# Optimization experiments

Hardware: AMD Instinct MI355X
Metric: run time of the kernel (lower is better)

Reference implementation:

```python
import jax, jax.numpy as jnp
import numpy as np


def _ln(x, g, b, eps=1e-5):
    m = jnp.mean(x, axis=-1, keepdims=True)
    v = jnp.var(x, axis=-1, keepdims=True)  # biased var, matches torch LayerNorm
    return (x - m) / jnp.sqrt(v + eps) * g + b


def setup_inputs() -> dict:
    key = jax.random.key(0)
    ks = jax.random.split(key, 10)
    B, S, T, D, F = 4, 8, 1024, 768, 16
    inp = {
        "target_hidden": jax.random.normal(ks[0], (B, T, D), jnp.float32),
        "support_hidden": jax.random.normal(ks[1], (B, S, T, D), jnp.float32),
        "support_token_mask": jax.random.bernoulli(ks[2], 0.8, (B, S, T)),
        "support_features": jax.random.normal(ks[3], (B, T, F), jnp.float32),
        # LayerNorm params
        "t_g": jnp.ones((D,), jnp.float32), "t_b": jnp.zeros((D,), jnp.float32),
        "s_g": jnp.ones((D,), jnp.float32), "s_b": jnp.zeros((D,), jnp.float32),
        "o_g": jnp.ones((D,), jnp.float32), "o_b": jnp.zeros((D,), jnp.float32),
        # score MLP: Linear(2D->D), GELU, Linear(D->1)
        "score_w1": jax.random.normal(ks[4], (2 * D, D), jnp.float32) * 0.02,
        "score_b1": jnp.zeros((D,), jnp.float32),
        "score_w2": jax.random.normal(ks[5], (D, 1), jnp.float32) * 0.02,
        "score_b2": jnp.zeros((1,), jnp.float32),
        # gate MLP: Linear(2D+F->D), GELU, Linear(D->1), Sigmoid
        "gate_w1": jax.random.normal(ks[6], (2 * D + F, D), jnp.float32) * 0.02,
        "gate_b1": jnp.zeros((D,), jnp.float32),
        "gate_w2": jax.random.normal(ks[7], (D, 1), jnp.float32) * 0.02,
        "gate_b2": jnp.zeros((1,), jnp.float32),
    }
    return inp


def reference(target_hidden, support_hidden, support_token_mask, support_features,
              t_g, t_b, s_g, s_b, o_g, o_b,
              score_w1, score_b1, score_w2, score_b2,
              gate_w1, gate_b1, gate_w2, gate_b2):
    D = target_hidden.shape[-1]
    mask = support_token_mask  # (B,S,T) bool

    th = _ln(target_hidden, t_g, t_b)        # (B,T,D)
    sh = _ln(support_hidden, s_g, s_b)       # (B,S,T,D)

    # score MLP on concat([target_expanded, support], -1) == split-weight form
    h = (jnp.einsum('btd,df->btf', th, score_w1[:D])[:, None, :, :]
         + jnp.einsum('bstd,df->bstf', sh, score_w1[D:]) + score_b1)  # (B,S,T,D)
    h = jax.nn.gelu(h, approximate=False)
    scores = jnp.einsum('bstd,d->bst', h, score_w2[:, 0]) + score_b2[0]  # (B,S,T)

    scores = jnp.where(mask, scores, -10000.0)
    w = jax.nn.softmax(scores, axis=1)
    w = w * mask.astype(w.dtype)
    w = w / jnp.clip(jnp.sum(w, axis=1, keepdims=True), 1e-8)

    summary = jnp.einsum('bst,bstd->btd', w, sh)  # (B,T,D)
    has_support = jnp.any(mask, axis=1)           # (B,T)
    summary = jnp.where(has_support[..., None], summary, 0.0)

    gcat = jnp.concatenate([th, summary, support_features], axis=-1)  # (B,T,2D+F)
    g = jax.nn.gelu(gcat @ gate_w1 + gate_b1, approximate=False)
    gate = jax.nn.sigmoid(g @ gate_w2 + gate_b2)  # (B,T,1)

    fused = gate * summary + (1.0 - gate) * th    # dropout is identity in eval
    out = _ln(th + fused, o_g, o_b)
    return out, gate.squeeze(-1)
```

## Files before the change

kernel.cpp:

```cpp
#include <hip/hip_runtime.h>
#include <hip/hip_bf16.h>

#define D768 768

typedef __attribute__((ext_vector_type(8))) short short8;
typedef __attribute__((ext_vector_type(4))) float f32x4;

__device__ __forceinline__ unsigned short f2bf(float f){
  union { float f; unsigned u; } v; v.f = f;
  unsigned r = v.u + 0x7FFFu + ((v.u >> 16) & 1u);
  return (unsigned short)(r >> 16);
}
__device__ __forceinline__ float bf2f(unsigned short u){
  union { unsigned u; float f; } v; v.u = ((unsigned)u) << 16;
  return v.f;
}
__device__ __forceinline__ float gelu_f(float x){
  float y = fabsf(x) * 0.7071067811865475f;
  float t = __builtin_amdgcn_rcpf(fmaf(0.3275911f, y, 1.0f));
  float p = fmaf(fmaf(fmaf(fmaf(1.061405429f, t, -1.453152027f), t, 1.421413741f),
                      t, -0.284496736f), t, 0.254829592f) * t;
  float e = __expf(-y * y);
  float erf_abs = fmaf(-p, e, 1.0f);
  float erfv = copysignf(erf_abs, x);
  return 0.5f * x * (1.0f + erfv);
}
__device__ __forceinline__ void gload16(const void* g, void* l){
  __builtin_amdgcn_global_load_lds((const __attribute__((address_space(1))) void*)g,
                                   (__attribute__((address_space(3))) void*)l, 16, 0, 0);
}

__global__ __launch_bounds__(256)
void k_mega(const float* __restrict__ target, const float* __restrict__ support,
            const float* __restrict__ t_g, const float* __restrict__ t_b,
            const float* __restrict__ s_g, const float* __restrict__ s_b,
            float* __restrict__ th, unsigned short* __restrict__ gcat,
            unsigned short* __restrict__ sh,
            const float* __restrict__ sw1, const float* __restrict__ gw1,
            unsigned short* __restrict__ WtA, unsigned short* __restrict__ WtB,
            unsigned short* __restrict__ WtG,
            float* __restrict__ scores, const float* __restrict__ sb2,
            float* __restrict__ gacc, const float* __restrict__ gb2,
            const unsigned char* __restrict__ m, int* __restrict__ flag){
  int blk = blockIdx.x;
  int t = threadIdx.x;
  if (blk < 128){
    int i = blk * 256 + t;
    if (i < 32768) scores[i] = sb2[0];
    if (i < 4096)  gacc[i]   = gb2[0];
    if (blk == 0){
      __shared__ int s;
      if (t == 0) s = 0;
      __syncthreads();
      int nz = 0;
      for (int j = t; j < 2048; j += 256) nz += (m[4*j+1] != 0);
      atomicAdd(&s, nz);
      __syncthreads();
      if (t == 0) *flag = (s == 0) ? 1 : 0;
    }
    return;
  }
  if (blk < 2456){
    int tile = blk - 128;
    const float* W; unsigned short* Wt; int Kin, Kpad;
    if (tile < 576)      { W = sw1;              Wt = WtA; Kin = 768;  Kpad = 768;  }
    else if (tile < 1152){ W = sw1 + 768ull*768; Wt = WtB; Kin = 768;  Kpad = 768;  tile -= 576; }
    else                 { W = gw1;              Wt = WtG; Kin = 1552; Kpad = 1568; tile -= 1152; }
    int ntk = Kpad >> 5;
    int k0 = (tile % ntk) << 5, n0 = (tile / ntk) << 5;
    __shared__ float ts[32][33];
    int tx = t & 31, ty = t >> 5;
    #pragma unroll
    for (int r = 0; r < 4; ++r){
      int k = k0 + ty + r*8;
      ts[ty + r*8][tx] = (k < Kin) ? W[(size_t)k * D768 + n0 + tx] : 0.f;
    }
    __syncthreads();
    #pragma unroll
    for (int r = 0; r < 4; ++r){
      int n = n0 + ty + r*8;
      Wt[(size_t)n * Kpad + k0 + tx] = f2bf(ts[tx][ty + r*8]);
    }
    return;
  }
  bool isT = blk < 3480;
  int row = (isT ? (blk - 2456) : (blk - 3480)) * 4 + (t >> 6);
  int lane = t & 63;
  const float* xr = (isT ? target : support) + (size_t)row * D768;
  float4 v0 = *(const float4*)(xr + lane*4);
  float4 v1 = *(const float4*)(xr + 256 + lane*4);
  float4 v2 = *(const float4*)(xr + 512 + lane*4);
  float s  = v0.x+v0.y+v0.z+v0.w + v1.x+v1.y+v1.z+v1.w + v2.x+v2.y+v2.z+v2.w;
  float ss = v0.x*v0.x+v0.y*v0.y+v0.z*v0.z+v0.w*v0.w
           + v1.x*v1.x+v1.y*v1.y+v1.z*v1.z+v1.w*v1.w
           + v2.x*v2.x+v2.y*v2.y+v2.z*v2.z+v2.w*v2.w;
  #pragma unroll
  for (int o = 32; o; o >>= 1){ s += __shfl_xor(s, o); ss += __shfl_xor(ss, o); }
  float mean = s * (1.f/768.f);
  float var  = ss * (1.f/768.f) - mean*mean;
  float rstd = rsqrtf(var + 1e-5f);
  const float* gg = isT ? t_g : s_g;
  const float* bb = isT ? t_b : s_b;
  #pragma unroll
  for (int k = 0; k < 3; ++k){
    int c = lane*4 + k*256;
    float4 v = (k==0) ? v0 : (k==1) ? v1 : v2;
    float4 gv = *(const float4*)(gg + c);
    float4 bv = *(const float4*)(bb + c);
    float o0 = (v.x-mean)*rstd*gv.x + bv.x;
    float o1 = (v.y-mean)*rstd*gv.y + bv.y;
    float o2 = (v.z-mean)*rstd*gv.z + bv.z;
    float o3 = (v.w-mean)*rstd*gv.w + bv.w;
    ushort4 ub; ub.x=f2bf(o0); ub.y=f2bf(o1); ub.z=f2bf(o2); ub.w=f2bf(o3);
    if (isT){
      float4 ov; ov.x=o0; ov.y=o1; ov.z=o2; ov.w=o3;
      *(float4*)(th + (size_t)row * D768 + c) = ov;
      *(ushort4*)(gcat + (size_t)row * 1568 + c) = ub;
    } else {
      *(ushort4*)(sh + (size_t)row * D768 + c) = ub;
    }
  }
}

template<int MODE, int BN>
__launch_bounds__(256)
__global__ void k_gemm(const unsigned short* __restrict__ A, int lda,
                       const unsigned short* __restrict__ Bt, int ldb,
                       int ksteps, int ntn,
                       const float* __restrict__ tproj,
                       const float* __restrict__ b1,
                       const float* __restrict__ w2,
                       float* __restrict__ out){
  constexpr int NJ  = BN / 32;
  constexpr int BCH = BN / 64;
  __shared__ __align__(16) unsigned short As[3][128*32];
  __shared__ __align__(16) unsigned short Bs[3][BN*32];
  const int cpx = gridDim.x >> 3;
  const int logical = ((int)blockIdx.x & 7) * cpx + ((int)blockIdx.x >> 3);
  const int m0 = (logical / ntn) * 128, n0 = (logical % ntn) * BN;
  const int t = threadIdx.x, lane = t & 63, w = t >> 6;
  const int wrow = (w >> 1) * 64, wcol = (w & 1) * (BN/2);
  const int lo16 = lane & 15;
  const int hs = ((lane >> 4) ^ ((lo16 >> 1) & 3)) * 8;
  const int crow = lane >> 2;
  const int cseg = (((lane & 3) ^ ((lane >> 3) & 3)) * 8);
  const unsigned short* ga = A  + (size_t)(m0 + w*32 + crow) * lda + cseg;
  const unsigned short* gb = Bt + (size_t)(n0 + w*(BN/4) + crow) * ldb + cseg;
  f32x4 acc[4][NJ] = {};

#define STAGEK(BUF, KS) do {                                                   \
    const unsigned short* gak_ = ga + (size_t)(KS)*32;                         \
    const unsigned short* gbk_ = gb + (size_t)(KS)*32;                         \
    _Pragma("unroll")                                                          \
    for (int c = 0; c < 2; ++c)                                                \
      gload16(gak_ + (size_t)(c*16)*lda, &As[BUF][w*1024 + c*512]);            \
    _Pragma("unroll")                                                          \
    for (int c = 0; c < BCH; ++c)                                              \
      gload16(gbk_ + (size_t)(c*16)*ldb, &Bs[BUF][w*(BN/4)*32 + c*512]);       \
  } while (0)

#define COMPUTEK(BUF) do {                                                     \
    const unsigned short* pa_ = &As[BUF][(wrow + lo16)*32 + hs];               \
    const unsigned short* pb_ = &Bs[BUF][(wcol + lo16)*32 + hs];               \
    short8 af_[4], bf_[NJ];                                                    \
    _Pragma("unroll")                                                          \
    for (int i = 0; i < 4; ++i) af_[i] = *(const short8*)(pa_ + i*16*32);      \
    _Pragma("unroll")                                                          \
    for (int j = 0; j < NJ; ++j) bf_[j] = *(const short8*)(pb_ + j*16*32);     \
    __builtin_amdgcn_s_setprio(1);                                             \
    _Pragma("unroll")                                                          \
    for (int i = 0; i < 4; ++i)                                                \
      _Pragma("unroll")                                                        \
      for (int j = 0; j < NJ; ++j)                                             \
        acc[i][j] = __builtin_amdgcn_mfma_f32_16x16x32_bf16(af_[i], bf_[j], acc[i][j], 0, 0, 0); \
    __builtin_amdgcn_s_setprio(0);                                             \
  } while (0)

#define WAITN(n) asm volatile("s_waitcnt vmcnt(" #n ")" ::: "memory")

  {
    int pro = ksteps < 2 ? ksteps : 2;
    for (int p = 0; p < pro; ++p) STAGEK(p, p);
  }
  for (int ks = 0; ks < ksteps; ++ks){
    int rem = ksteps - ks;
    if (rem >= 2){ if constexpr (BCH == 2) WAITN(4); else WAITN(3); }
    else WAITN(0);
    __builtin_amdgcn_s_barrier();
    __builtin_amdgcn_sched_barrier(0);
    if (ks + 2 < ksteps) STAGEK((ks + 2) % 3, ks + 2);
    COMPUTEK(ks % 3);
  }
#undef STAGEK
#undef COMPUTEK
#undef WAITN

  if (MODE == 0){
    #pragma unroll
    for (int i = 0; i < 4; ++i)
      #pragma unroll
      for (int reg = 0; reg < 4; ++reg){
        int row = m0 + wrow + i*16 + ((lane >> 4) << 2) + reg;
        float* orow = out + (size_t)row * D768 + n0 + wcol + (lane & 15);
        #pragma unroll
        for (int j = 0; j < NJ; ++j) orow[j*16] = acc[i][j][reg];
      }
  } else {
    #pragma unroll
    for (int i = 0; i < 4; ++i)
      #pragma unroll
      for (int reg = 0; reg < 4; ++reg){
        int row = m0 + wrow + i*16 + ((lane >> 4) << 2) + reg;
        const float* tp = nullptr;
        if (MODE == 1){
          int trow = ((row >> 13) << 10) | (row & 1023);
          tp = tproj + (size_t)trow * D768;
        }
        float contrib = 0.f;
        #pragma unroll
        for (int j = 0; j < NJ; ++j){
          int n = n0 + wcol + j*16 + (lane & 15);
          float v = acc[i][j][reg] + b1[n];
          if (MODE == 1) v += tp[n];
          contrib += gelu_f(v) * w2[n];
        }
        for (int o = 8; o; o >>= 1) contrib += __shfl_xor(contrib, o);
        if ((lane & 15) == 0) atomicAdd(&out[row], contrib);
      }
  }
}

__launch_bounds__(512)
__global__ void k_gemm8(const unsigned short* __restrict__ A, int lda,
                        const unsigned short* __restrict__ Bt, int ldb,
                        int ksteps, int ntn,
                        const float* __restrict__ tproj,
                        const float* __restrict__ b1,
                        const float* __restrict__ w2,
                        float* __restrict__ out){
  __shared__ __align__(16) unsigned short As[3][256*32];
  __shared__ __align__(16) unsigned short Bs[3][128*32];
  const int cpx = gridDim.x >> 3;
  const int logical = ((int)blockIdx.x & 7) * cpx + ((int)blockIdx.x >> 3);
  const int m0 = (logical / ntn) * 256, n0 = (logical % ntn) * 128;
  const int t = threadIdx.x, lane = t & 63, w = t >> 6;
  const int wrow = (w >> 1) * 64, wcol = (w & 1) * 64;
  const int lo16 = lane & 15;
  const int hs = ((lane >> 4) ^ ((lo16 >> 1) & 3)) * 8;
  const int crow = lane >> 2;
  const int cseg = (((lane & 3) ^ ((lane >> 3) & 3)) * 8);
  const unsigned short* ga = A  + (size_t)(m0 + w*32 + crow) * lda + cseg;
  const unsigned short* gb = Bt + (size_t)(n0 + w*16 + crow) * ldb + cseg;
  f32x4 acc[4][4] = {};

#define STAGEK(BUF, KS) do {                                                   \
    const unsigned short* gak_ = ga + (size_t)(KS)*32;                         \
    gload16(gak_,                    &As[BUF][w*1024]);                        \
    gload16(gak_ + (size_t)16*lda,   &As[BUF][w*1024 + 512]);                  \
    gload16(gb + (size_t)(KS)*32,    &Bs[BUF][w*512]);                         \
  } while (0)

#define COMPUTEK(BUF) do {                                                     \
    const unsigned short* pa_ = &As[BUF][(wrow + lo16)*32 + hs];               \
    const unsigned short* pb_ = &Bs[BUF][(wcol + lo16)*32 + hs];               \
    short8 af_[4], bf_[4];                                                     \
    _Pragma("unroll")                                                          \
    for (int i = 0; i < 4; ++i) af_[i] = *(const short8*)(pa_ + i*16*32);      \
    _Pragma("unroll")                                                          \
    for (int j = 0; j < 4; ++j) bf_[j] = *(const short8*)(pb_ + j*16*32);      \
    __builtin_amdgcn_s_setprio(1);                                             \
    _Pragma("unroll")                                                          \
    for (int i = 0; i < 4; ++i)                                                \
      _Pragma("unroll")                                                        \
      for (int j = 0; j < 4; ++j)                                              \
        acc[i][j] = __builtin_amdgcn_mfma_f32_16x16x32_bf16(af_[i], bf_[j], acc[i][j], 0, 0, 0); \
    __builtin_amdgcn_s_setprio(0);                                             \
  } while (0)

#define WAITN(n) asm volatile("s_waitcnt vmcnt(" #n ")" ::: "memory")

  {
    int pro = ksteps < 2 ? ksteps : 2;
    for (int p = 0; p < pro; ++p) STAGEK(p, p);
  }
  for (int ks = 0; ks < ksteps; ++ks){
    int rem = ksteps - ks;
    if (rem >= 2) WAITN(3);
    else WAITN(0);
    __builtin_amdgcn_s_barrier();
    __builtin_amdgcn_sched_barrier(0);
    if (ks + 2 < ksteps) STAGEK((ks + 2) % 3, ks + 2);
    COMPUTEK(ks % 3);
  }
#undef STAGEK
#undef COMPUTEK
#undef WAITN

  float b1v[4], w2v[4];
  #pragma unroll
  for (int j = 0; j < 4; ++j){
    int n = n0 + wcol + j*16 + lo16;
    b1v[j] = b1[n]; w2v[j] = w2[n];
  }
  #pragma unroll
  for (int i = 0; i < 4; ++i)
    #pragma unroll
    for (int reg = 0; reg < 4; ++reg){
      int row = m0 + wrow + i*16 + ((lane >> 4) << 2) + reg;
      int trow = ((row >> 13) << 10) | (row & 1023);
      const float* tp = tproj + (size_t)trow * D768;
      float contrib = 0.f;
      #pragma unroll
      for (int j = 0; j < 4; ++j){
        int n = n0 + wcol + j*16 + lo16;
        float v = acc[i][j][reg] + b1v[j] + tp[n];
        contrib += gelu_f(v) * w2v[j];
      }
      for (int o = 8; o; o >>= 1) contrib += __shfl_xor(contrib, o);
      if (lo16 == 0) atomicAdd(&out[row], contrib);
    }
}

__launch_bounds__(512)
__global__ void k_gemm8g(const unsigned short* __restrict__ A, int lda,
                         const unsigned short* __restrict__ Bt, int ldb,
                         int ksteps, int ntn,
                         const float* __restrict__ b1,
                         const float* __restrict__ w2,
                         float* __restrict__ out){
  __shared__ __align__(16) unsigned short As[3][128*32];
  __shared__ __align__(16) unsigned short Bs[3][64*32];
  const int cpx = gridDim.x >> 3;
  const int logical = ((int)blockIdx.x & 7) * cpx + ((int)blockIdx.x >> 3);
  const int m0 = (logical / ntn) * 128, n0 = (logical % ntn) * 64;
  const int t = threadIdx.x, lane = t & 63, w = t >> 6;
  const int wrow = (w >> 2) * 64, wcol = (w & 3) * 16;
  const int lo16 = lane & 15;
  const int hs = ((lane >> 4) ^ ((lo16 >> 1) & 3)) * 8;
  const int crow = lane >> 2;
  const int cseg = (((lane & 3) ^ ((lane >> 3) & 3)) * 8);
  const unsigned short* ga = A  + (size_t)(m0 + w*16 + crow) * lda + cseg;
  const unsigned short* gb = Bt + (size_t)(n0 + w*16 + crow) * ldb + cseg;
  f32x4 acc[4] = {};

#define STAGEK(BUF, KS) do {                                                   \
    gload16(ga + (size_t)(KS)*32, &As[BUF][w*512]);                            \
    if (w < 4) gload16(gb + (size_t)(KS)*32, &Bs[BUF][w*512]);                 \
  } while (0)

#define COMPUTEK(BUF) do {                                                     \
    const unsigned short* pa_ = &As[BUF][(wrow + lo16)*32 + hs];               \
    const unsigned short* pb_ = &Bs[BUF][(wcol + lo16)*32 + hs];               \
    short8 af_[4], bf_;                                                        \
    _Pragma("unroll")                                                          \
    for (int i = 0; i < 4; ++i) af_[i] = *(const short8*)(pa_ + i*16*32);      \
    bf_ = *(const short8*)pb_;                                                 \
    __builtin_amdgcn_s_setprio(1);                                             \
    _Pragma("unroll")                                                          \
    for (int i = 0; i < 4; ++i)                                                \
      acc[i] = __builtin_amdgcn_mfma_f32_16x16x32_bf16(af_[i], bf_, acc[i], 0, 0, 0); \
    __builtin_amdgcn_s_setprio(0);                                             \
  } while (0)

#define WAITN(n) asm volatile("s_waitcnt vmcnt(" #n ")" ::: "memory")

  {
    int pro = ksteps < 2 ? ksteps : 2;
    for (int p = 0; p < pro; ++p) STAGEK(p, p);
  }
  for (int ks = 0; ks < ksteps; ++ks){
    int rem = ksteps - ks;
    if (rem >= 2){ if (w < 4) WAITN(2); else WAITN(1); }
    else WAITN(0);
    __builtin_amdgcn_s_barrier();
    __builtin_amdgcn_sched_barrier(0);
    if (ks + 2 < ksteps) STAGEK((ks + 2) % 3, ks + 2);
    COMPUTEK(ks % 3);
  }
#undef STAGEK
#undef COMPUTEK
#undef WAITN

  #pragma unroll
  for (int i = 0; i < 4; ++i)
    #pragma unroll
    for (int reg = 0; reg < 4; ++reg){
      int row = m0 + wrow + i*16 + ((lane >> 4) << 2) + reg;
      int n = n0 + wcol + lo16;
      float v = acc[i][reg] + b1[n];
      float contrib = gelu_f(v) * w2[n];
      for (int o = 8; o; o >>= 1) contrib += __shfl_xor(contrib, o);
      if (lo16 == 0) atomicAdd(&out[row], contrib);
    }
}

__global__ void k_smx(const float* __restrict__ scores, const void* __restrict__ maskp,
                      const int* __restrict__ flag, const unsigned short* __restrict__ sh,
                      const float* __restrict__ feat,
                      unsigned short* __restrict__ gcat){
  int bt = blockIdx.x;
  int b = bt >> 10, tt = bt & 1023;
  int t = threadIdx.x;
  int f = *flag;
  float sc[8], mk[8];
  #pragma unroll
  for (int s = 0; s < 8; ++s){
    size_t idx = ((size_t)(b*8 + s) << 10) + tt;
    bool m = f ? (((const int*)maskp)[idx] != 0)
               : (((const unsigned char*)maskp)[idx] != 0);
    mk[s] = m ? 1.f : 0.f;
    float v = scores[idx];
    sc[s] = m ? v : -10000.f;
  }
  float mx = sc[0];
  #pragma unroll
  for (int s = 1; s < 8; ++s) mx = fmaxf(mx, sc[s]);
  float e[8], sum = 0.f;
  #pragma unroll
  for (int s = 0; s < 8; ++s){ e[s] = __expf(sc[s] - mx); sum += e[s]; }
  float inv = 1.f / sum;
  float wv[8], sum2 = 0.f;
  #pragma unroll
  for (int s = 0; s < 8; ++s){ wv[s] = e[s] * inv * mk[s]; sum2 += wv[s]; }
  float inv2 = 1.f / fmaxf(sum2, 1e-8f);
  #pragma unroll
  for (int s = 0; s < 8; ++s) wv[s] *= inv2;
  float a0=0.f, a1=0.f, a2=0.f, a3=0.f;
  #pragma unroll
  for (int s = 0; s < 8; ++s){
    const unsigned short* p = sh + (((size_t)(b*8+s) << 10) + tt) * D768 + t*4;
    ushort4 u = *(const ushort4*)p;
    float ws = wv[s];
    a0 += ws * bf2f(u.x); a1 += ws * bf2f(u.y); a2 += ws * bf2f(u.z); a3 += ws * bf2f(u.w);
  }
  ushort4 ub; ub.x=f2bf(a0); ub.y=f2bf(a1); ub.z=f2bf(a2); ub.w=f2bf(a3);
  *(ushort4*)(gcat + (size_t)bt * 1568 + 768 + t*4) = ub;
  if (t < 8){
    int c = 1536 + t*4;
    float4 fv = make_float4(0.f, 0.f, 0.f, 0.f);
    if (c < 1552) fv = *(const float4*)(feat + (size_t)bt * 16 + (c - 1536));
    ushort4 uf; uf.x=f2bf(fv.x); uf.y=f2bf(fv.y); uf.z=f2bf(fv.z); uf.w=f2bf(fv.w);
    *(ushort4*)(gcat + (size_t)bt * 1568 + c) = uf;
  }
}

__global__ __launch_bounds__(256)
void k_final(const float* __restrict__ th, const unsigned short* __restrict__ gcat,
             const float* __restrict__ gacc, const float* __restrict__ og,
             const float* __restrict__ ob, float* __restrict__ out,
             float* __restrict__ outg){
  int row = blockIdx.x * 4 + (threadIdx.x >> 6);
  int lane = threadIdx.x & 63;
  float gv = 1.f / (1.f + __expf(-gacc[row]));
  if (lane == 0) outg[row] = gv;
  const float* tr = th + (size_t)row * D768;
  const unsigned short* sr = gcat + (size_t)row * 1568 + 768;
  float x[12];
  float s = 0.f, ss = 0.f;
  #pragma unroll
  for (int k = 0; k < 3; ++k){
    int c = lane*4 + k*256;
    float4 tv = *(const float4*)(tr + c);
    ushort4 su = *(const ushort4*)(sr + c);
    float v0 = (2.f-gv)*tv.x + gv*bf2f(su.x);
    float v1 = (2.f-gv)*tv.y + gv*bf2f(su.y);
    float v2 = (2.f-gv)*tv.z + gv*bf2f(su.z);
    float v3 = (2.f-gv)*tv.w + gv*bf2f(su.w);
    x[k*4+0]=v0; x[k*4+1]=v1; x[k*4+2]=v2; x[k*4+3]=v3;
    s += v0+v1+v2+v3;
    ss += v0*v0+v1*v1+v2*v2+v3*v3;
  }
  #pragma unroll
  for (int o = 32; o; o >>= 1){ s += __shfl_xor(s, o); ss += __shfl_xor(ss, o); }
  float mean = s*(1.f/768.f), var = ss*(1.f/768.f)-mean*mean;
  float rstd = rsqrtf(var + 1e-5f);
  #pragma unroll
  for (int k = 0; k < 3; ++k){
    int c = lane*4 + k*256;
    float4 gvv = *(const float4*)(og + c);
    float4 bvv = *(const float4*)(ob + c);
    float4 ov;
    ov.x = (x[k*4+0]-mean)*rstd*gvv.x + bvv.x;
    ov.y = (x[k*4+1]-mean)*rstd*gvv.y + bvv.y;
    ov.z = (x[k*4+2]-mean)*rstd*gvv.z + bvv.z;
    ov.w = (x[k*4+3]-mean)*rstd*gvv.w + bvv.w;
    *(float4*)(out + (size_t)row * D768 + c) = ov;
  }
}

extern "C" void kernel_launch(void* const* d_in, const int* in_sizes, int n_in,
                              void* d_out, int out_size, void* d_ws, size_t ws_size,
                              hipStream_t stream){
  const float* target = (const float*)d_in[0];
  const float* support= (const float*)d_in[1];
  const void*  maskp  = d_in[2];
  const float* feat   = (const float*)d_in[3];
  const float* t_g = (const float*)d_in[4];
  const float* t_b = (const float*)d_in[5];
  const float* s_g = (const float*)d_in[6];
  const float* s_b = (const float*)d_in[7];
  const float* o_g = (const float*)d_in[8];
  const float* o_b = (const float*)d_in[9];
  const float* sw1 = (const float*)d_in[10];
  const float* sb1 = (const float*)d_in[11];
  const float* sw2 = (const float*)d_in[12];
  const float* sb2 = (const float*)d_in[13];
  const float* gw1 = (const float*)d_in[14];
  const float* gb1 = (const float*)d_in[15];
  const float* gw2 = (const float*)d_in[16];
  const float* gb2 = (const float*)d_in[17];

  char* wsb = (char*)d_ws;
  size_t off = 0;
  auto alloc = [&](size_t bytes)->void*{
    void* p = wsb + off; off += (bytes + 255) & ~(size_t)255; return p;
  };
  float* th            = (float*)alloc(4096ull*768*4);
  unsigned short* sh   = (unsigned short*)alloc(32768ull*768*2);
  float* tproj         = (float*)alloc(4096ull*768*4);
  unsigned short* gcat = (unsigned short*)alloc(4096ull*1568*2);
  unsigned short* WtA  = (unsigned short*)alloc(768ull*768*2);
  unsigned short* WtB  = (unsigned short*)alloc(768ull*768*2);
  unsigned short* WtG  = (unsigned short*)alloc(768ull*1568*2);
  float* scores        = (float*)alloc(32768ull*4);
  float* gacc          = (float*)alloc(4096ull*4);
  int*   flag          = (int*)alloc(256);

  float* outm = (float*)d_out;
  float* outg = outm + 4096ull*768;

  k_mega<<<11672, 256, 0, stream>>>(target, support, t_g, t_b, s_g, s_b,
                                    th, gcat, sh, sw1, gw1, WtA, WtB, WtG,
                                    scores, sb2, gacc, gb2,
                                    (const unsigned char*)maskp, flag);
  k_gemm<0,64><<<384, 256, 0, stream>>>(gcat, 1568, WtA, 768, 24, 12,
                                        nullptr, nullptr, nullptr, tproj);
  k_gemm8<<<768, 512, 0, stream>>>(sh, 768, WtB, 768, 24, 6,
                                   tproj, sb1, sw2, scores);
  k_smx<<<4096, 192, 0, stream>>>(scores, maskp, flag, sh, feat, gcat);
  k_gemm8g<<<384, 512, 0, stream>>>(gcat, 1568, WtG, 1568, 49, 12,
                                    gb1, gw2, gacc);
  k_final<<<1024, 256, 0, stream>>>(th, gcat, gacc, o_g, o_b, outm, outg);
}
```

Measured before the change: 171.1 us.

## Rewrite score GEMM with 256x256 tiles and phased double-buffered pipeline

```diff
diff --git a/kernel.cpp b/kernel.cpp
--- a/kernel.cpp
+++ b/kernel.cpp
@@ -211,17 +211,11 @@
       #pragma unroll
       for (int reg = 0; reg < 4; ++reg){
         int row = m0 + wrow + i*16 + ((lane >> 4) << 2) + reg;
-        const float* tp = nullptr;
-        if (MODE == 1){
-          int trow = ((row >> 13) << 10) | (row & 1023);
-          tp = tproj + (size_t)trow * D768;
-        }
         float contrib = 0.f;
         #pragma unroll
         for (int j = 0; j < NJ; ++j){
           int n = n0 + wcol + j*16 + (lane & 15);
           float v = acc[i][j][reg] + b1[n];
-          if (MODE == 1) v += tp[n];
           contrib += gelu_f(v) * w2[n];
         }
         for (int o = 8; o; o >>= 1) contrib += __shfl_xor(contrib, o);
@@ -231,89 +225,94 @@
 }
 
 __launch_bounds__(512)
-__global__ void k_gemm8(const unsigned short* __restrict__ A, int lda,
+__global__ void k_score(const unsigned short* __restrict__ A, int lda,
                         const unsigned short* __restrict__ Bt, int ldb,
-                        int ksteps, int ntn,
+                        int ntn,
                         const float* __restrict__ tproj,
                         const float* __restrict__ b1,
                         const float* __restrict__ w2,
                         float* __restrict__ out){
-  __shared__ __align__(16) unsigned short As[3][256*32];
-  __shared__ __align__(16) unsigned short Bs[3][128*32];
+  __shared__ __align__(16) unsigned short Ah[2][2][256*32];
+  __shared__ __align__(16) unsigned short Bh[2][2][256*32];
   const int cpx = gridDim.x >> 3;
   const int logical = ((int)blockIdx.x & 7) * cpx + ((int)blockIdx.x >> 3);
-  const int m0 = (logical / ntn) * 256, n0 = (logical % ntn) * 128;
+  const int m0 = (logical / ntn) * 256, n0 = (logical % ntn) * 256;
   const int t = threadIdx.x, lane = t & 63, w = t >> 6;
-  const int wrow = (w >> 1) * 64, wcol = (w & 1) * 64;
+  const int wr = w >> 2, wc = w & 3;
   const int lo16 = lane & 15;
   const int hs = ((lane >> 4) ^ ((lo16 >> 1) & 3)) * 8;
-  const int crow = lane >> 2;
   const int cseg = (((lane & 3) ^ ((lane >> 3) & 3)) * 8);
-  const unsigned short* ga = A  + (size_t)(m0 + w*32 + crow) * lda + cseg;
-  const unsigned short* gb = Bt + (size_t)(n0 + w*16 + crow) * ldb + cseg;
-  f32x4 acc[4][4] = {};
-
-#define STAGEK(BUF, KS) do {                                                   \
-    const unsigned short* gak_ = ga + (size_t)(KS)*32;                         \
-    gload16(gak_,                    &As[BUF][w*1024]);                        \
-    gload16(gak_ + (size_t)16*lda,   &As[BUF][w*1024 + 512]);                  \
-    gload16(gb + (size_t)(KS)*32,    &Bs[BUF][w*512]);                         \
-  } while (0)
-
-#define COMPUTEK(BUF) do {                                                     \
-    const unsigned short* pa_ = &As[BUF][(wrow + lo16)*32 + hs];               \
-    const unsigned short* pb_ = &Bs[BUF][(wcol + lo16)*32 + hs];               \
-    short8 af_[4], bf_[4];                                                     \
-    _Pragma("unroll")                                                          \
-    for (int i = 0; i < 4; ++i) af_[i] = *(const short8*)(pa_ + i*16*32);      \
-    _Pragma("unroll")                                                          \
-    for (int j = 0; j < 4; ++j) bf_[j] = *(const short8*)(pb_ + j*16*32);      \
+  const unsigned short* ga = A  + (size_t)(m0 + w*32 + (lane >> 2)) * lda + cseg;
+  const unsigned short* gb = Bt + (size_t)(n0 + w*32 + (lane >> 2)) * ldb + cseg;
+  f32x4 acc[8][4] = {};
+
+#define PHASE(B, S, RH, T) do {                                                \
+    short8 afr[4], bfr[4];                                                     \
+    const unsigned short* pa_ = &Ah[B][S][((wr*128 + (RH)*64 + lo16)*32)] + hs;\
+    const unsigned short* pb_ = &Bh[B][S][((wc*64 + lo16)*32)] + hs;           \
+    _Pragma("unroll")                                                          \
+    for (int i = 0; i < 4; ++i) afr[i] = *(const short8*)(pa_ + i*512);        \
+    _Pragma("unroll")                                                          \
+    for (int j = 0; j < 4; ++j) bfr[j] = *(const short8*)(pb_ + j*512);        \
+    if ((T) + 1 < 12){                                                         \
+      const unsigned short* gs_ = ((RH) == 0 ? ga : gb) + (size_t)(((T)+1)*64 + (S)*32); \
+      unsigned short* ld_ = ((RH) == 0 ? &Ah[(B)^1][S][w*1024] : &Bh[(B)^1][S][w*1024]); \
+      gload16(gs_, ld_);                                                       \
+      gload16(gs_ + (size_t)16*((RH)==0 ? lda : ldb), ld_ + 512);              \
+    }                                                                          \
+    __builtin_amdgcn_s_barrier();                                              \
+    asm volatile("s_waitcnt lgkmcnt(0)" ::: "memory");                         \
+    __builtin_amdgcn_sched_barrier(0);                                         \
     __builtin_amdgcn_s_setprio(1);                                             \
     _Pragma("unroll")                                                          \
     for (int i = 0; i < 4; ++i)                                                \
       _Pragma("unroll")                                                        \
       for (int j = 0; j < 4; ++j)                                              \
-        acc[i][j] = __builtin_amdgcn_mfma_f32_16x16x32_bf16(af_[i], bf_[j], acc[i][j], 0, 0, 0); \
+        acc[(RH)*4+i][j] = __builtin_amdgcn_mfma_f32_16x16x32_bf16(afr[i], bfr[j], acc[(RH)*4+i][j], 0, 0, 0); \
     __builtin_amdgcn_s_setprio(0);                                             \
+    if (RH){                                                                   \
+      if ((T) == 11) asm volatile("s_waitcnt vmcnt(0)" ::: "memory");          \
+      else           asm volatile("s_waitcnt vmcnt(4)" ::: "memory");          \
+    }                                                                          \
+    __builtin_amdgcn_s_barrier();                                              \
   } while (0)
 
-#define WAITN(n) asm volatile("s_waitcnt vmcnt(" #n ")" ::: "memory")
-
-  {
-    int pro = ksteps < 2 ? ksteps : 2;
-    for (int p = 0; p < pro; ++p) STAGEK(p, p);
-  }
-  for (int ks = 0; ks < ksteps; ++ks){
-    int rem = ksteps - ks;
-    if (rem >= 2) WAITN(3);
-    else WAITN(0);
-    __builtin_amdgcn_s_barrier();
-    __builtin_amdgcn_sched_barrier(0);
-    if (ks + 2 < ksteps) STAGEK((ks + 2) % 3, ks + 2);
-    COMPUTEK(ks % 3);
-  }
-#undef STAGEK
-#undef COMPUTEK
-#undef WAITN
+  gload16(ga,                       &Ah[0][0][w*1024]);
+  gload16(ga + (size_t)16*lda,      &Ah[0][0][w*1024 + 512]);
+  gload16(gb,                       &Bh[0][0][w*1024]);
+  gload16(gb + (size_t)16*ldb,      &Bh[0][0][w*1024 + 512]);
+  gload16(ga + 32,                  &Ah[0][1][w*1024]);
+  gload16(ga + 32 + (size_t)16*lda, &Ah[0][1][w*1024 + 512]);
+  gload16(gb + 32,                  &Bh[0][1][w*1024]);
+  gload16(gb + 32 + (size_t)16*ldb, &Bh[0][1][w*1024 + 512]);
+  asm volatile("s_waitcnt vmcnt(4)" ::: "memory");
+  __builtin_amdgcn_s_barrier();
+  #pragma unroll 1
+  for (int tp = 0; tp < 6; ++tp){
+    int t0 = 2*tp, t1 = 2*tp + 1;
+    PHASE(0,0,0,t0); PHASE(0,0,1,t0); PHASE(0,1,0,t0); PHASE(0,1,1,t0);
+    PHASE(1,0,0,t1); PHASE(1,0,1,t1); PHASE(1,1,0,t1); PHASE(1,1,1,t1);
+  }
+#undef PHASE
 
   float b1v[4], w2v[4];
   #pragma unroll
   for (int j = 0; j < 4; ++j){
-    int n = n0 + wcol + j*16 + lo16;
+    int n = n0 + wc*64 + j*16 + lo16;
     b1v[j] = b1[n]; w2v[j] = w2[n];
   }
   #pragma unroll
-  for (int i = 0; i < 4; ++i)
+  for (int rf = 0; rf < 8; ++rf)
     #pragma unroll
     for (int reg = 0; reg < 4; ++reg){
-      int row = m0 + wrow + i*16 + ((lane >> 4) << 2) + reg;
+      int row = m0 + wr*128 + rf*16 + ((lane >> 4) << 2) + reg;
       int trow = ((row >> 13) << 10) | (row & 1023);
       const float* tp = tproj + (size_t)trow * D768;
       float contrib = 0.f;
       #pragma unroll
       for (int j = 0; j < 4; ++j){
-        int n = n0 + wcol + j*16 + lo16;
-        float v = acc[i][j][reg] + b1v[j] + tp[n];
+        int n = n0 + wc*64 + j*16 + lo16;
+        float v = acc[rf][j][reg] + b1v[j] + tp[n];
         contrib += gelu_f(v) * w2v[j];
       }
       for (int o = 8; o; o >>= 1) contrib += __shfl_xor(contrib, o);
@@ -535,7 +534,7 @@
                                     (const unsigned char*)maskp, flag);
   k_gemm<0,64><<<384, 256, 0, stream>>>(gcat, 1568, WtA, 768, 24, 12,
                                         nullptr, nullptr, nullptr, tproj);
-  k_gemm8<<<768, 512, 0, stream>>>(sh, 768, WtB, 768, 24, 6,
+  k_score<<<384, 512, 0, stream>>>(sh, 768, WtB, 768, 3,
                                    tproj, sb1, sw2, scores);
   k_smx<<<4096, 192, 0, stream>>>(scores, maskp, flag, sh, feat, gcat);
   k_gemm8g<<<384, 512, 0, stream>>>(gcat, 1568, WtG, 1568, 49, 12,
```

New measurement: 202.3 us. 1.18x slower.

## Overlap target projection GEMM with support LayerNorm in one launch

Applied to the files above, without the earlier changes.

```diff
diff --git a/kernel.cpp b/kernel.cpp
--- a/kernel.cpp
+++ b/kernel.cpp
@@ -31,17 +31,15 @@
 }
 
 __global__ __launch_bounds__(256)
-void k_mega(const float* __restrict__ target, const float* __restrict__ support,
-            const float* __restrict__ t_g, const float* __restrict__ t_b,
-            const float* __restrict__ s_g, const float* __restrict__ s_b,
-            float* __restrict__ th, unsigned short* __restrict__ gcat,
-            unsigned short* __restrict__ sh,
-            const float* __restrict__ sw1, const float* __restrict__ gw1,
-            unsigned short* __restrict__ WtA, unsigned short* __restrict__ WtB,
-            unsigned short* __restrict__ WtG,
-            float* __restrict__ scores, const float* __restrict__ sb2,
-            float* __restrict__ gacc, const float* __restrict__ gb2,
-            const unsigned char* __restrict__ m, int* __restrict__ flag){
+void k_pre(const float* __restrict__ target,
+           const float* __restrict__ t_g, const float* __restrict__ t_b,
+           float* __restrict__ th, unsigned short* __restrict__ gcat,
+           const float* __restrict__ sw1, const float* __restrict__ gw1,
+           unsigned short* __restrict__ WtA, unsigned short* __restrict__ WtB,
+           unsigned short* __restrict__ WtG,
+           float* __restrict__ scores, const float* __restrict__ sb2,
+           float* __restrict__ gacc, const float* __restrict__ gb2,
+           const unsigned char* __restrict__ m, int* __restrict__ flag){
   int blk = blockIdx.x;
   int t = threadIdx.x;
   if (blk < 128){
@@ -83,10 +81,9 @@
     }
     return;
   }
-  bool isT = blk < 3480;
-  int row = (isT ? (blk - 2456) : (blk - 3480)) * 4 + (t >> 6);
+  int row = (blk - 2456) * 4 + (t >> 6);
   int lane = t & 63;
-  const float* xr = (isT ? target : support) + (size_t)row * D768;
+  const float* xr = target + (size_t)row * D768;
   float4 v0 = *(const float4*)(xr + lane*4);
   float4 v1 = *(const float4*)(xr + 256 + lane*4);
   float4 v2 = *(const float4*)(xr + 512 + lane*4);
@@ -99,134 +96,126 @@
   float mean = s * (1.f/768.f);
   float var  = ss * (1.f/768.f) - mean*mean;
   float rstd = rsqrtf(var + 1e-5f);
-  const float* gg = isT ? t_g : s_g;
-  const float* bb = isT ? t_b : s_b;
   #pragma unroll
   for (int k = 0; k < 3; ++k){
     int c = lane*4 + k*256;
     float4 v = (k==0) ? v0 : (k==1) ? v1 : v2;
-    float4 gv = *(const float4*)(gg + c);
-    float4 bv = *(const float4*)(bb + c);
+    float4 gv = *(const float4*)(t_g + c);
+    float4 bv = *(const float4*)(t_b + c);
+    float o0 = (v.x-mean)*rstd*gv.x + bv.x;
+    float o1 = (v.y-mean)*rstd*gv.y + bv.y;
+    float o2 = (v.z-mean)*rstd*gv.z + bv.z;
+    float o3 = (v.w-mean)*rstd*gv.w + bv.w;
+    float4 ov; ov.x=o0; ov.y=o1; ov.z=o2; ov.w=o3;
+    *(float4*)(th + (size_t)row * D768 + c) = ov;
+    ushort4 ub; ub.x=f2bf(o0); ub.y=f2bf(o1); ub.z=f2bf(o2); ub.w=f2bf(o3);
+    *(ushort4*)(gcat + (size_t)row * 1568 + c) = ub;
+  }
+}
+
+__global__ __launch_bounds__(256)
+void k_slntp(const float* __restrict__ support,
+             const float* __restrict__ s_g, const float* __restrict__ s_b,
+             unsigned short* __restrict__ sh,
+             const unsigned short* __restrict__ gcat,
+             const unsigned short* __restrict__ WtA,
+             float* __restrict__ tproj){
+  __shared__ __align__(16) unsigned short As[3][128*32];
+  __shared__ __align__(16) unsigned short Bs[3][64*32];
+  int blk = blockIdx.x;
+  int t = threadIdx.x;
+  if (blk < 384){
+    const int logical = (blk & 7) * 48 + (blk >> 3);
+    const int m0 = (logical / 12) * 128, n0 = (logical % 12) * 64;
+    const int lane = t & 63, w = t >> 6;
+    const int wrow = (w >> 1) * 64, wcol = (w & 1) * 32;
+    const int lo16 = lane & 15;
+    const int hs = ((lane >> 4) ^ ((lo16 >> 1) & 3)) * 8;
+    const int crow = lane >> 2;
+    const int cseg = (((lane & 3) ^ ((lane >> 3) & 3)) * 8);
+    const unsigned short* ga = gcat + (size_t)(m0 + w*32 + crow) * 1568 + cseg;
+    const unsigned short* gb = WtA  + (size_t)(n0 + w*16 + crow) * 768 + cseg;
+    f32x4 acc[4][2] = {};
+
+#define STAGEK(BUF, KS) do {                                                   \
+    const unsigned short* gak_ = ga + (size_t)(KS)*32;                         \
+    gload16(gak_,                  &As[BUF][w*1024]);                          \
+    gload16(gak_ + (size_t)16*1568,&As[BUF][w*1024 + 512]);                    \
+    if (w < 4) gload16(gb + (size_t)(KS)*32 + 0, &Bs[BUF][w*512]);             \
+  } while (0)
+
+#define COMPUTEK(BUF) do {                                                     \
+    const unsigned short* pa_ = &As[BUF][(wrow + lo16)*32 + hs];               \
+    const unsigned short* pb_ = &Bs[BUF][(wcol + lo16)*32 + hs];               \
+    short8 af_[4], bf_[2];                                                     \
+    _Pragma("unroll")                                                          \
+    for (int i = 0; i < 4; ++i) af_[i] = *(const short8*)(pa_ + i*16*32);      \
+    _Pragma("unroll")                                                          \
+    for (int j = 0; j < 2; ++j) bf_[j] = *(const short8*)(pb_ + j*16*32);      \
+    __builtin_amdgcn_s_setprio(1);                                             \
+    _Pragma("unroll")                                                          \
+    for (int i = 0; i < 4; ++i)                                                \
+      _Pragma("unroll")                                                        \
+      for (int j = 0; j < 2; ++j)                                              \
+        acc[i][j] = __builtin_amdgcn_mfma_f32_16x16x32_bf16(af_[i], bf_[j], acc[i][j], 0, 0, 0); \
+    __builtin_amdgcn_s_setprio(0);                                             \
+  } while (0)
+
+#define WAITN(n) asm volatile("s_waitcnt vmcnt(" #n ")" ::: "memory")
+
+    STAGEK(0, 0);
+    STAGEK(1, 1);
+    for (int ks = 0; ks < 24; ++ks){
+      int rem = 24 - ks;
+      if (rem >= 2){ if (w < 4) WAITN(3); else WAITN(2); }
+      else WAITN(0);
+      __builtin_amdgcn_s_barrier();
+      __builtin_amdgcn_sched_barrier(0);
+      if (ks + 2 < 24) STAGEK((ks + 2) % 3, ks + 2);
+      COMPUTEK(ks % 3);
+    }
+#undef STAGEK
+#undef COMPUTEK
+#undef WAITN
+
+    #pragma unroll
+    for (int i = 0; i < 4; ++i)
+      #pragma unroll
+      for (int reg = 0; reg < 4; ++reg){
+        int row = m0 + wrow + i*16 + ((lane >> 4) << 2) + reg;
+        float* orow = tproj + (size_t)row * D768 + n0 + wcol + lo16;
+        #pragma unroll
+        for (int j = 0; j < 2; ++j) orow[j*16] = acc[i][j][reg];
+      }
+    return;
+  }
+  int row = (blk - 384) * 4 + (t >> 6);
+  int lane = t & 63;
+  const float* xr = support + (size_t)row * D768;
+  float4 v0 = *(const float4*)(xr + lane*4);
+  float4 v1 = *(const float4*)(xr + 256 + lane*4);
+  float4 v2 = *(const float4*)(xr + 512 + lane*4);
+  float s  = v0.x+v0.y+v0.z+v0.w + v1.x+v1.y+v1.z+v1.w + v2.x+v2.y+v2.z+v2.w;
+  float ss = v0.x*v0.x+v0.y*v0.y+v0.z*v0.z+v0.w*v0.w
+           + v1.x*v1.x+v1.y*v1.y+v1.z*v1.z+v1.w*v1.w
+           + v2.x*v2.x+v2.y*v2.y+v2.z*v2.z+v2.w*v2.w;
+  #pragma unroll
+  for (int o = 32; o; o >>= 1){ s += __shfl_xor(s, o); ss += __shfl_xor(ss, o); }
+  float mean = s * (1.f/768.f);
+  float var  = ss * (1.f/768.f) - mean*mean;
+  float rstd = rsqrtf(var + 1e-5f);
+  #pragma unroll
+  for (int k = 0; k < 3; ++k){
+    int c = lane*4 + k*256;
+    float4 v = (k==0) ? v0 : (k==1) ? v1 : v2;
+    float4 gv = *(const float4*)(s_g + c);
+    float4 bv = *(const float4*)(s_b + c);
     float o0 = (v.x-mean)*rstd*gv.x + bv.x;
     float o1 = (v.y-mean)*rstd*gv.y + bv.y;
     float o2 = (v.z-mean)*rstd*gv.z + bv.z;
     float o3 = (v.w-mean)*rstd*gv.w + bv.w;
     ushort4 ub; ub.x=f2bf(o0); ub.y=f2bf(o1); ub.z=f2bf(o2); ub.w=f2bf(o3);
-    if (isT){
-      float4 ov; ov.x=o0; ov.y=o1; ov.z=o2; ov.w=o3;
-      *(float4*)(th + (size_t)row * D768 + c) = ov;
-      *(ushort4*)(gcat + (size_t)row * 1568 + c) = ub;
-    } else {
-      *(ushort4*)(sh + (size_t)row * D768 + c) = ub;
-    }
-  }
-}
-
-template<int MODE, int BN>
-__launch_bounds__(256)
-__global__ void k_gemm(const unsigned short* __restrict__ A, int lda,
-                       const unsigned short* __restrict__ Bt, int ldb,
-                       int ksteps, int ntn,
-                       const float* __restrict__ tproj,
-                       const float* __restrict__ b1,
-                       const float* __restrict__ w2,
-                       float* __restrict__ out){
-  constexpr int NJ  = BN / 32;
-  constexpr int BCH = BN / 64;
-  __shared__ __align__(16) unsigned short As[3][128*32];
-  __shared__ __align__(16) unsigned short Bs[3][BN*32];
-  const int cpx = gridDim.x >> 3;
-  const int logical = ((int)blockIdx.x & 7) * cpx + ((int)blockIdx.x >> 3);
-  const int m0 = (logical / ntn) * 128, n0 = (logical % ntn) * BN;
-  const int t = threadIdx.x, lane = t & 63, w = t >> 6;
-  const int wrow = (w >> 1) * 64, wcol = (w & 1) * (BN/2);
-  const int lo16 = lane & 15;
-  const int hs = ((lane >> 4) ^ ((lo16 >> 1) & 3)) * 8;
-  const int crow = lane >> 2;
-  const int cseg = (((lane & 3) ^ ((lane >> 3) & 3)) * 8);
-  const unsigned short* ga = A  + (size_t)(m0 + w*32 + crow) * lda + cseg;
-  const unsigned short* gb = Bt + (size_t)(n0 + w*(BN/4) + crow) * ldb + cseg;
-  f32x4 acc[4][NJ] = {};
-
-#define STAGEK(BUF, KS) do {                                                   \
-    const unsigned short* gak_ = ga + (size_t)(KS)*32;                         \
-    const unsigned short* gbk_ = gb + (size_t)(KS)*32;                         \
-    _Pragma("unroll")                                                          \
-    for (int c = 0; c < 2; ++c)                                                \
-      gload16(gak_ + (size_t)(c*16)*lda, &As[BUF][w*1024 + c*512]);            \
-    _Pragma("unroll")                                                          \
-    for (int c = 0; c < BCH; ++c)                                              \
-      gload16(gbk_ + (size_t)(c*16)*ldb, &Bs[BUF][w*(BN/4)*32 + c*512]);       \
-  } while (0)
-
-#define COMPUTEK(BUF) do {                                                     \
-    const unsigned short* pa_ = &As[BUF][(wrow + lo16)*32 + hs];               \
-    const unsigned short* pb_ = &Bs[BUF][(wcol + lo16)*32 + hs];               \
-    short8 af_[4], bf_[NJ];                                                    \
-    _Pragma("unroll")                                                          \
-    for (int i = 0; i < 4; ++i) af_[i] = *(const short8*)(pa_ + i*16*32);      \
-    _Pragma("unroll")                                                          \
-    for (int j = 0; j < NJ; ++j) bf_[j] = *(const short8*)(pb_ + j*16*32);     \
-    __builtin_amdgcn_s_setprio(1);                                             \
-    _Pragma("unroll")                                                          \
-    for (int i = 0; i < 4; ++i)                                                \
-      _Pragma("unroll")                                                        \
-      for (int j = 0; j < NJ; ++j)                                             \
-        acc[i][j] = __builtin_amdgcn_mfma_f32_16x16x32_bf16(af_[i], bf_[j], acc[i][j], 0, 0, 0); \
-    __builtin_amdgcn_s_setprio(0);                                             \
-  } while (0)
-
-#define WAITN(n) asm volatile("s_waitcnt vmcnt(" #n ")" ::: "memory")
-
-  {
-    int pro = ksteps < 2 ? ksteps : 2;
-    for (int p = 0; p < pro; ++p) STAGEK(p, p);
-  }
-  for (int ks = 0; ks < ksteps; ++ks){
-    int rem = ksteps - ks;
-    if (rem >= 2){ if constexpr (BCH == 2) WAITN(4); else WAITN(3); }
-    else WAITN(0);
-    __builtin_amdgcn_s_barrier();
-    __builtin_amdgcn_sched_barrier(0);
-    if (ks + 2 < ksteps) STAGEK((ks + 2) % 3, ks + 2);
-    COMPUTEK(ks % 3);
-  }
-#undef STAGEK
-#undef COMPUTEK
-#undef WAITN
-
-  if (MODE == 0){
-    #pragma unroll
-    for (int i = 0; i < 4; ++i)
-      #pragma unroll
-      for (int reg = 0; reg < 4; ++reg){
-        int row = m0 + wrow + i*16 + ((lane >> 4) << 2) + reg;
-        float* orow = out + (size_t)row * D768 + n0 + wcol + (lane & 15);
-        #pragma unroll
-        for (int j = 0; j < NJ; ++j) orow[j*16] = acc[i][j][reg];
-      }
-  } else {
-    #pragma unroll
-    for (int i = 0; i < 4; ++i)
-      #pragma unroll
-      for (int reg = 0; reg < 4; ++reg){
-        int row = m0 + wrow + i*16 + ((lane >> 4) << 2) + reg;
-        const float* tp = nullptr;
-        if (MODE == 1){
-          int trow = ((row >> 13) << 10) | (row & 1023);
-          tp = tproj + (size_t)trow * D768;
-        }
-        float contrib = 0.f;
-        #pragma unroll
-        for (int j = 0; j < NJ; ++j){
-          int n = n0 + wcol + j*16 + (lane & 15);
-          float v = acc[i][j][reg] + b1[n];
-          if (MODE == 1) v += tp[n];
-          contrib += gelu_f(v) * w2[n];
-        }
-        for (int o = 8; o; o >>= 1) contrib += __shfl_xor(contrib, o);
-        if ((lane & 15) == 0) atomicAdd(&out[row], contrib);
-      }
+    *(ushort4*)(sh + (size_t)row * D768 + c) = ub;
   }
 }
 
@@ -529,12 +518,11 @@
   float* outm = (float*)d_out;
   float* outg = outm + 4096ull*768;
 
-  k_mega<<<11672, 256, 0, stream>>>(target, support, t_g, t_b, s_g, s_b,
-                                    th, gcat, sh, sw1, gw1, WtA, WtB, WtG,
-                                    scores, sb2, gacc, gb2,
-                                    (const unsigned char*)maskp, flag);
-  k_gemm<0,64><<<384, 256, 0, stream>>>(gcat, 1568, WtA, 768, 24, 12,
-                                        nullptr, nullptr, nullptr, tproj);
+  k_pre<<<3480, 256, 0, stream>>>(target, t_g, t_b, th, gcat,
+                                  sw1, gw1, WtA, WtB, WtG,
+                                  scores, sb2, gacc, gb2,
+                                  (const unsigned char*)maskp, flag);
+  k_slntp<<<8576, 256, 0, stream>>>(support, s_g, s_b, sh, gcat, WtA, tproj);
   k_gemm8<<<768, 512, 0, stream>>>(sh, 768, WtB, 768, 24, 6,
                                    tproj, sb1, sw2, scores);
   k_smx<<<4096, 192, 0, stream>>>(scores, maskp, flag, sh, feat, gcat);
```

Result: faster. 160.9 us (-5.9%).
